# Optimization experiments

Hardware: AMD Instinct MI355X
Metric: run time of the kernel (lower is better)

Reference implementation:

```python
import jax, jax.numpy as jnp
import numpy as np

B, N, C = 32, 577, 768
H = 12
D = C // H
HID = 4 * C
EPS = 1e-5


def setup_inputs() -> dict:
    key = jax.random.key(0)
    ks = jax.random.split(key, 12)
    s = 0.02
    return {
        "x": jax.random.normal(ks[0], (B, N, C), dtype=jnp.float32),
        "ln1_g": jnp.ones((C,), jnp.float32),
        "ln1_b": jnp.zeros((C,), jnp.float32),
        "qkv_w": jax.random.normal(ks[1], (C, 3 * C), jnp.float32) * s,
        "qkv_b": jnp.zeros((3 * C,), jnp.float32),
        "proj_w": jax.random.normal(ks[2], (C, C), jnp.float32) * s,
        "proj_b": jnp.zeros((C,), jnp.float32),
        "ln2_g": jnp.ones((C,), jnp.float32),
        "ln2_b": jnp.zeros((C,), jnp.float32),
        "fc1_w": jax.random.normal(ks[3], (C, HID), jnp.float32) * s,
        "fc1_b": jnp.zeros((HID,), jnp.float32),
        "fc2_w": jax.random.normal(ks[4], (HID, C), jnp.float32) * s,
        "fc2_b": jnp.zeros((C,), jnp.float32),
    }


def _layernorm(x, g, b):
    mu = jnp.mean(x, axis=-1, keepdims=True)
    var = jnp.mean(jnp.square(x - mu), axis=-1, keepdims=True)
    return (x - mu) * jax.lax.rsqrt(var + EPS) * g + b


def reference(x, ln1_g, ln1_b, qkv_w, qkv_b, proj_w, proj_b,
              ln2_g, ln2_b, fc1_w, fc1_b, fc2_w, fc2_b):
    b, n, c = x.shape
    # --- MSA branch ---
    h = _layernorm(x, ln1_g, ln1_b)
    qkv = h @ qkv_w + qkv_b                      # [b, n, 3c]
    qkv = qkv.reshape(b, n, 3, H, D).transpose(2, 0, 3, 1, 4)  # [3, b, h, n, d]
    q, k, v = qkv[0], qkv[1], qkv[2]
    scale = D ** -0.5
    attn = jnp.einsum('bhqd,bhkd->bhqk', q, k) * scale
    attn = jax.nn.softmax(attn, axis=-1)
    o = jnp.einsum('bhqk,bhkd->bhqd', attn, v)   # [b, h, n, d]
    o = o.transpose(0, 2, 1, 3).reshape(b, n, c)
    o = o @ proj_w + proj_b
    x = x + o
    # --- MLP branch ---
    h = _layernorm(x, ln2_g, ln2_b)
    h = jax.nn.gelu(h @ fc1_w + fc1_b, approximate=False)  # torch nn.GELU = exact erf
    h = h @ fc2_w + fc2_b
    return x + h
```

## Files before the change

### kernel.cpp

```cpp
#include <hip/hip_runtime.h>

typedef unsigned short u16;
typedef short short8 __attribute__((ext_vector_type(8)));
typedef float f32x4 __attribute__((ext_vector_type(4)));

#define MM 18464
#define CC 768
#define NTOK 577

__device__ __forceinline__ u16 f2bf(float f) {
    unsigned u = __builtin_bit_cast(unsigned, f);
    u += 0x7fffu + ((u >> 16) & 1u);
    return (u16)(u >> 16);
}

__device__ __forceinline__ void gload16(const void* g, void* lds) {
    __builtin_amdgcn_global_load_lds(
        (const __attribute__((address_space(1))) unsigned*)g,
        (__attribute__((address_space(3))) unsigned*)lds,
        16, 0, 0);
}

__global__ __launch_bounds__(256) void convT(const float* __restrict__ src,
                                             u16* __restrict__ dst, int K, int N) {
    __shared__ float tile[32][33];
    const int k0 = blockIdx.x * 32, n0 = blockIdx.y * 32;
    const int tx = threadIdx.x & 31, ty = threadIdx.x >> 5;
#pragma unroll
    for (int i = 0; i < 32; i += 8)
        tile[ty + i][tx] = src[(size_t)(k0 + ty + i) * N + n0 + tx];
    __syncthreads();
#pragma unroll
    for (int i = 0; i < 32; i += 8)
        dst[(size_t)(n0 + ty + i) * K + k0 + tx] = f2bf(tile[tx][ty + i]);
}

__global__ __launch_bounds__(192) void ln_k(const float* __restrict__ x,
                                            const float* __restrict__ g,
                                            const float* __restrict__ bt,
                                            u16* __restrict__ out) {
    const int row = blockIdx.x, t = threadIdx.x;
    const float4 v = reinterpret_cast<const float4*>(x + (size_t)row * 768)[t];
    float s = v.x + v.y + v.z + v.w;
    float s2 = v.x * v.x + v.y * v.y + v.z * v.z + v.w * v.w;
#pragma unroll
    for (int off = 32; off > 0; off >>= 1) {
        s += __shfl_down(s, off);
        s2 += __shfl_down(s2, off);
    }
    __shared__ float red[6];
    if ((t & 63) == 0) { red[t >> 6] = s; red[3 + (t >> 6)] = s2; }
    __syncthreads();
    const float S = red[0] + red[1] + red[2];
    const float S2 = red[3] + red[4] + red[5];
    const float mu = S * (1.f / 768.f);
    const float var = S2 * (1.f / 768.f) - mu * mu;
    const float rs = rsqrtf(var + 1e-5f);
    const float4 gg = reinterpret_cast<const float4*>(g)[t];
    const float4 bb = reinterpret_cast<const float4*>(bt)[t];
    ushort4 r;
    r.x = f2bf((v.x - mu) * rs * gg.x + bb.x);
    r.y = f2bf((v.y - mu) * rs * gg.y + bb.y);
    r.z = f2bf((v.z - mu) * rs * gg.z + bb.z);
    r.w = f2bf((v.w - mu) * rs * gg.w + bb.w);
    reinterpret_cast<ushort4*>(out + (size_t)row * 768)[t] = r;
}

template <int MODE>
__global__ __launch_bounds__(256) void gemm_k(const u16* __restrict__ A,
                                              const u16* __restrict__ BT,
                                              const float* __restrict__ bias,
                                              const float* __restrict__ resid,
                                              void* __restrict__ outp,
                                              int M, int N, int K) {
    __shared__ u16 As[128 * 32];
    __shared__ u16 Bs[128 * 32];
    const int t = threadIdx.x;
    const int wid = t >> 6, lane = t & 63;
    const int l15 = lane & 15, lg = lane >> 4;
    const int m0 = blockIdx.x * 128, n0 = blockIdx.y * 128;
    const int wr = wid >> 1, wc = wid & 1;

    f32x4 acc[4][4] = {};

    const int srow = t >> 2;
    const int sk = (t & 3) * 8;
    const size_t a0 = (size_t)min(m0 + srow, M - 1) * K + sk;
    const size_t a1 = (size_t)min(m0 + srow + 64, M - 1) * K + sk;
    const size_t b0 = (size_t)(n0 + srow) * K + sk;
    const size_t b1 = (size_t)(n0 + srow + 64) * K + sk;
    u16* ldsA = As + wid * 512;
    u16* ldsB = Bs + wid * 512;

    for (int k0 = 0; k0 < K; k0 += 32) {
        gload16(A + a0 + k0, ldsA);
        gload16(A + a1 + k0, ldsA + 2048);
        gload16(BT + b0 + k0, ldsB);
        gload16(BT + b1 + k0, ldsB + 2048);
        __syncthreads();
        short8 af[4], bf[4];
#pragma unroll
        for (int fr = 0; fr < 4; ++fr)
            af[fr] = *(const short8*)&As[(wr * 64 + fr * 16 + l15) * 32 + lg * 8];
#pragma unroll
        for (int fc = 0; fc < 4; ++fc)
            bf[fc] = *(const short8*)&Bs[(wc * 64 + fc * 16 + l15) * 32 + lg * 8];
#pragma unroll
        for (int fr = 0; fr < 4; ++fr)
#pragma unroll
            for (int fc = 0; fc < 4; ++fc)
                acc[fr][fc] = __builtin_amdgcn_mfma_f32_16x16x32_bf16(
                    af[fr], bf[fc], acc[fr][fc], 0, 0, 0);
        __syncthreads();
    }

    float bcol[4];
#pragma unroll
    for (int fc = 0; fc < 4; ++fc) bcol[fc] = bias[n0 + wc * 64 + fc * 16 + l15];
#pragma unroll
    for (int fr = 0; fr < 4; ++fr) {
#pragma unroll
        for (int reg = 0; reg < 4; ++reg) {
            const int row = m0 + wr * 64 + fr * 16 + lg * 4 + reg;
            if (row < M) {
#pragma unroll
                for (int fc = 0; fc < 4; ++fc) {
                    const int col = n0 + wc * 64 + fc * 16 + l15;
                    float v = acc[fr][fc][reg] + bcol[fc];
                    if (MODE == 2) v = 0.5f * v * (1.0f + erff(v * 0.70710678118f));
                    if (MODE == 1 || MODE == 3) v += resid[(size_t)row * N + col];
                    if (MODE == 0 || MODE == 2)
                        ((u16*)outp)[(size_t)row * N + col] = f2bf(v);
                    else
                        ((float*)outp)[(size_t)row * N + col] = v;
                }
            }
        }
    }
}

__global__ __launch_bounds__(256) void attn_k(const u16* __restrict__ qkv,
                                              u16* __restrict__ o) {
    const int qt = blockIdx.x;
    const int bh = blockIdx.y;
    const int b = bh / 12, h = bh % 12;
    const int t = threadIdx.x, wid = t >> 6, lane = t & 63;
    const int l15 = lane & 15, lg = lane >> 4;
    const size_t base = ((size_t)b * NTOK) * 2304 + (size_t)h * 64;

    __shared__ u16 Ks[64 * 64], Vs[64 * 64], Ps[64 * 64];

    int qrow = qt * 64 + wid * 16 + l15;
    qrow = min(qrow, NTOK - 1);
    const u16* Qp = qkv + base + (size_t)qrow * 2304 + lg * 8;
    const short8 qf0 = *(const short8*)(Qp);
    const short8 qf1 = *(const short8*)(Qp + 32);

    f32x4 oacc[4] = {};
    float m_run[4], l_run[4];
#pragma unroll
    for (int j = 0; j < 4; ++j) { m_run[j] = -1e30f; l_run[j] = 0.f; }

    const int srow = t >> 3;
    const int sd = (t & 7) * 8;
    u16* ldsK = Ks + wid * 512;
    u16* ldsV = Vs + wid * 512;

    for (int kt = 0; kt < 10; ++kt) {
        const int n0t = kt * 64;
        const int r0 = min(n0t + srow, NTOK - 1);
        const int r1 = min(n0t + srow + 32, NTOK - 1);
        gload16(qkv + base + 768 + (size_t)r0 * 2304 + sd, ldsK);
        gload16(qkv + base + 768 + (size_t)r1 * 2304 + sd, ldsK + 2048);
        gload16(qkv + base + 1536 + (size_t)r0 * 2304 + sd, ldsV);
        gload16(qkv + base + 1536 + (size_t)r1 * 2304 + sd, ldsV + 2048);
        __syncthreads();

        f32x4 s[4];
#pragma unroll
        for (int fc = 0; fc < 4; ++fc) {
            f32x4 a_ = {};
            const short8 kf0 = *(const short8*)&Ks[(fc * 16 + l15) * 64 + lg * 8];
            const short8 kf1 = *(const short8*)&Ks[(fc * 16 + l15) * 64 + 32 + lg * 8];
            a_ = __builtin_amdgcn_mfma_f32_16x16x32_bf16(qf0, kf0, a_, 0, 0, 0);
            a_ = __builtin_amdgcn_mfma_f32_16x16x32_bf16(qf1, kf1, a_, 0, 0, 0);
            s[fc] = a_;
        }
#pragma unroll
        for (int fc = 0; fc < 4; ++fc) {
            const bool valid = (n0t + fc * 16 + l15) < NTOK;
#pragma unroll
            for (int j = 0; j < 4; ++j)
                s[fc][j] = valid ? s[fc][j] * 0.125f : -1e30f;
        }
        float mt[4];
#pragma unroll
        for (int j = 0; j < 4; ++j)
            mt[j] = fmaxf(fmaxf(s[0][j], s[1][j]), fmaxf(s[2][j], s[3][j]));
#pragma unroll
        for (int off = 1; off < 16; off <<= 1)
#pragma unroll
            for (int j = 0; j < 4; ++j) mt[j] = fmaxf(mt[j], __shfl_xor(mt[j], off));
        float mn[4], alpha[4];
#pragma unroll
        for (int j = 0; j < 4; ++j) {
            mn[j] = fmaxf(m_run[j], mt[j]);
            alpha[j] = __expf(m_run[j] - mn[j]);
            m_run[j] = mn[j];
        }
        float lsum[4] = {0.f, 0.f, 0.f, 0.f};
#pragma unroll
        for (int fc = 0; fc < 4; ++fc)
#pragma unroll
            for (int j = 0; j < 4; ++j) {
                const float p = __expf(s[fc][j] - mn[j]);
                s[fc][j] = p;
                lsum[j] += p;
            }
#pragma unroll
        for (int off = 1; off < 16; off <<= 1)
#pragma unroll
            for (int j = 0; j < 4; ++j) lsum[j] += __shfl_xor(lsum[j], off);
#pragma unroll
        for (int j = 0; j < 4; ++j) l_run[j] = l_run[j] * alpha[j] + lsum[j];
#pragma unroll
        for (int fc = 0; fc < 4; ++fc)
#pragma unroll
            for (int j = 0; j < 4; ++j) oacc[fc][j] *= alpha[j];

#pragma unroll
        for (int fc = 0; fc < 4; ++fc)
#pragma unroll
            for (int j = 0; j < 4; ++j)
                Ps[(wid * 16 + lg * 4 + j) * 64 + fc * 16 + l15] = f2bf(s[fc][j]);
        asm volatile("s_waitcnt lgkmcnt(0)" ::: "memory");

#pragma unroll
        for (int c = 0; c < 2; ++c) {
            const short8 pf = *(const short8*)&Ps[(wid * 16 + l15) * 64 + c * 32 + lg * 8];
#pragma unroll
            for (int fc = 0; fc < 4; ++fc) {
                short8 vf;
#pragma unroll
                for (int j = 0; j < 8; ++j)
                    vf[j] = (short)Vs[(c * 32 + lg * 8 + j) * 64 + fc * 16 + l15];
                oacc[fc] = __builtin_amdgcn_mfma_f32_16x16x32_bf16(pf, vf, oacc[fc], 0, 0, 0);
            }
        }
        __syncthreads();
    }

#pragma unroll
    for (int j = 0; j < 4; ++j) {
        const int row = qt * 64 + wid * 16 + lg * 4 + j;
        if (row < NTOK) {
            const float inv = 1.0f / l_run[j];
#pragma unroll
            for (int fc = 0; fc < 4; ++fc)
                o[((size_t)(b * NTOK + row)) * 768 + h * 64 + fc * 16 + l15] =
                    f2bf(oacc[fc][j] * inv);
        }
    }
}

extern "C" void kernel_launch(void* const* d_in, const int* in_sizes, int n_in,
                              void* d_out, int out_size, void* d_ws, size_t ws_size,
                              hipStream_t stream) {
    const float* x      = (const float*)d_in[0];
    const float* ln1_g  = (const float*)d_in[1];
    const float* ln1_b  = (const float*)d_in[2];
    const float* qkv_w  = (const float*)d_in[3];
    const float* qkv_b  = (const float*)d_in[4];
    const float* proj_w = (const float*)d_in[5];
    const float* proj_b = (const float*)d_in[6];
    const float* ln2_g  = (const float*)d_in[7];
    const float* ln2_b  = (const float*)d_in[8];
    const float* fc1_w  = (const float*)d_in[9];
    const float* fc1_b  = (const float*)d_in[10];
    const float* fc2_w  = (const float*)d_in[11];
    const float* fc2_b  = (const float*)d_in[12];
    float* out = (float*)d_out;

    char* ws = (char*)d_ws;
    size_t off = 0;
    u16* WQ  = (u16*)(ws + off); off += (size_t)2304 * 768 * 2;
    u16* WP  = (u16*)(ws + off); off += (size_t)768 * 768 * 2;
    u16* W1  = (u16*)(ws + off); off += (size_t)3072 * 768 * 2;
    u16* W2  = (u16*)(ws + off); off += (size_t)768 * 3072 * 2;
    u16* LN1 = (u16*)(ws + off); off += (size_t)MM * 768 * 2;
    u16* QKV = (u16*)(ws + off); off += (size_t)MM * 2304 * 2;
    u16* OB  = (u16*)(ws + off); off += (size_t)MM * 768 * 2;
    float* X1 = (float*)(ws + off); off += (size_t)MM * 768 * 4;
    u16* LN2 = (u16*)(ws + off); off += (size_t)MM * 768 * 2;
    u16* HID = LN1;

    convT<<<dim3(24, 72), 256, 0, stream>>>(qkv_w, WQ, 768, 2304);
    convT<<<dim3(24, 24), 256, 0, stream>>>(proj_w, WP, 768, 768);
    convT<<<dim3(24, 96), 256, 0, stream>>>(fc1_w, W1, 768, 3072);
    convT<<<dim3(96, 24), 256, 0, stream>>>(fc2_w, W2, 3072, 768);

    ln_k<<<MM, 192, 0, stream>>>(x, ln1_g, ln1_b, LN1);
    gemm_k<0><<<dim3(145, 18), 256, 0, stream>>>(LN1, WQ, qkv_b, nullptr, QKV,
                                                 MM, 2304, 768);
    attn_k<<<dim3(10, 384), 256, 0, stream>>>(QKV, OB);
    gemm_k<1><<<dim3(145, 6), 256, 0, stream>>>(OB, WP, proj_b, x, X1,
                                                MM, 768, 768);
    ln_k<<<MM, 192, 0, stream>>>(X1, ln2_g, ln2_b, LN2);
    gemm_k<2><<<dim3(145, 24), 256, 0, stream>>>(LN2, W1, fc1_b, nullptr, HID,
                                                 MM, 3072, 768);
    gemm_k<3><<<dim3(145, 6), 256, 0, stream>>>(HID, W2, fc2_b, X1, out,
                                                MM, 768, 3072);
}
```

Before: 891.8 us.

## Double-buffer GEMM LDS, add XCD swizzle, transpose V with XOR-swizzled attention LDS

The GEMM kernel now double-buffers its LDS tiles so the next K-slice's global-to-LDS load is issued before computing on the current slice. Both GEMM and attention remap block indices across the eight XCDs to improve L2 locality. In attention, K and P use XOR-swizzled LDS layouts to reduce bank conflicts, and V is stored transposed so the PV MFMA operand becomes a single 16-byte vector read instead of eight scalar LDS reads. The tradeoffs are twice the GEMM LDS footprint and V staging through registers rather than direct global-to-LDS loads.

```diff
diff --git a/kernel.cpp b/kernel.cpp
--- a/kernel.cpp
+++ b/kernel.cpp
@@ -5,7 +5,6 @@
 typedef float f32x4 __attribute__((ext_vector_type(4)));
 
 #define MM 18464
-#define CC 768
 #define NTOK 577
 
 __device__ __forceinline__ u16 f2bf(float f) {
@@ -19,6 +18,15 @@
         (const __attribute__((address_space(1))) unsigned*)g,
         (__attribute__((address_space(3))) unsigned*)lds,
         16, 0, 0);
+}
+
+__device__ __forceinline__ int2 xcd_swz(int gx, int gy) {
+    const int nwg = gx * gy;
+    const int flat = blockIdx.x + blockIdx.y * gx;
+    const int q = nwg >> 3, r = nwg & 7;
+    const int xcd = flat & 7, lid = flat >> 3;
+    const int w = (xcd < r ? xcd * (q + 1) : r * (q + 1) + (xcd - r) * q) + lid;
+    int2 o; o.x = w % gx; o.y = w / gx; return o;
 }
 
 __global__ __launch_bounds__(256) void convT(const float* __restrict__ src,
@@ -73,12 +81,13 @@
                                               const float* __restrict__ resid,
                                               void* __restrict__ outp,
                                               int M, int N, int K) {
-    __shared__ u16 As[128 * 32];
-    __shared__ u16 Bs[128 * 32];
+    __shared__ u16 As[2][128 * 32];
+    __shared__ u16 Bs[2][128 * 32];
     const int t = threadIdx.x;
     const int wid = t >> 6, lane = t & 63;
     const int l15 = lane & 15, lg = lane >> 4;
-    const int m0 = blockIdx.x * 128, n0 = blockIdx.y * 128;
+    const int2 sw = xcd_swz(gridDim.x, gridDim.y);
+    const int m0 = sw.x * 128, n0 = sw.y * 128;
     const int wr = wid >> 1, wc = wid & 1;
 
     f32x4 acc[4][4] = {};
@@ -89,30 +98,41 @@
     const size_t a1 = (size_t)min(m0 + srow + 64, M - 1) * K + sk;
     const size_t b0 = (size_t)(n0 + srow) * K + sk;
     const size_t b1 = (size_t)(n0 + srow + 64) * K + sk;
-    u16* ldsA = As + wid * 512;
-    u16* ldsB = Bs + wid * 512;
-
-    for (int k0 = 0; k0 < K; k0 += 32) {
-        gload16(A + a0 + k0, ldsA);
-        gload16(A + a1 + k0, ldsA + 2048);
-        gload16(BT + b0 + k0, ldsB);
-        gload16(BT + b1 + k0, ldsB + 2048);
-        __syncthreads();
-        short8 af[4], bf[4];
+    const int wo = wid * 512;
+
+    auto stage = [&](int buf, int k0) {
+        gload16(A + a0 + k0, &As[buf][wo]);
+        gload16(A + a1 + k0, &As[buf][wo + 2048]);
+        gload16(BT + b0 + k0, &Bs[buf][wo]);
+        gload16(BT + b1 + k0, &Bs[buf][wo + 2048]);
+    };
+    auto compute = [&](int buf) {
+        short8 af[4], bfr[4];
 #pragma unroll
         for (int fr = 0; fr < 4; ++fr)
-            af[fr] = *(const short8*)&As[(wr * 64 + fr * 16 + l15) * 32 + lg * 8];
+            af[fr] = *(const short8*)&As[buf][(wr * 64 + fr * 16 + l15) * 32 + lg * 8];
 #pragma unroll
         for (int fc = 0; fc < 4; ++fc)
-            bf[fc] = *(const short8*)&Bs[(wc * 64 + fc * 16 + l15) * 32 + lg * 8];
+            bfr[fc] = *(const short8*)&Bs[buf][(wc * 64 + fc * 16 + l15) * 32 + lg * 8];
 #pragma unroll
         for (int fr = 0; fr < 4; ++fr)
 #pragma unroll
             for (int fc = 0; fc < 4; ++fc)
                 acc[fr][fc] = __builtin_amdgcn_mfma_f32_16x16x32_bf16(
-                    af[fr], bf[fc], acc[fr][fc], 0, 0, 0);
+                    af[fr], bfr[fc], acc[fr][fc], 0, 0, 0);
+    };
+
+    stage(0, 0);
+    __syncthreads();
+    int cur = 0;
+    const int nk = K >> 5;
+    for (int kt = 1; kt < nk; ++kt) {
+        stage(cur ^ 1, kt * 32);
+        compute(cur);
         __syncthreads();
-    }
+        cur ^= 1;
+    }
+    compute(cur);
 
     float bcol[4];
 #pragma unroll
@@ -141,14 +161,15 @@
 
 __global__ __launch_bounds__(256) void attn_k(const u16* __restrict__ qkv,
                                               u16* __restrict__ o) {
-    const int qt = blockIdx.x;
-    const int bh = blockIdx.y;
+    const int2 sw = xcd_swz(10, 384);
+    const int qt = sw.x;
+    const int bh = sw.y;
     const int b = bh / 12, h = bh % 12;
     const int t = threadIdx.x, wid = t >> 6, lane = t & 63;
     const int l15 = lane & 15, lg = lane >> 4;
     const size_t base = ((size_t)b * NTOK) * 2304 + (size_t)h * 64;
 
-    __shared__ u16 Ks[64 * 64], Vs[64 * 64], Ps[64 * 64];
+    __shared__ u16 Ks[64 * 64], VT[64 * 64], Ps[64 * 64];
 
     int qrow = qt * 64 + wid * 16 + l15;
     qrow = min(qrow, NTOK - 1);
@@ -162,26 +183,34 @@
     for (int j = 0; j < 4; ++j) { m_run[j] = -1e30f; l_run[j] = 0.f; }
 
     const int srow = t >> 3;
-    const int sd = (t & 7) * 8;
+    const int cchunk = t & 7;
+    const int ksd = (cchunk ^ (srow & 7)) * 8;
     u16* ldsK = Ks + wid * 512;
-    u16* ldsV = Vs + wid * 512;
+    const int vs0 = ((srow >> 3) ^ cchunk) * 8 + (srow & 7);
+    const int vs1 = (((srow >> 3) + 4) ^ cchunk) * 8 + (srow & 7);
 
     for (int kt = 0; kt < 10; ++kt) {
         const int n0t = kt * 64;
         const int r0 = min(n0t + srow, NTOK - 1);
         const int r1 = min(n0t + srow + 32, NTOK - 1);
-        gload16(qkv + base + 768 + (size_t)r0 * 2304 + sd, ldsK);
-        gload16(qkv + base + 768 + (size_t)r1 * 2304 + sd, ldsK + 2048);
-        gload16(qkv + base + 1536 + (size_t)r0 * 2304 + sd, ldsV);
-        gload16(qkv + base + 1536 + (size_t)r1 * 2304 + sd, ldsV + 2048);
+        gload16(qkv + base + 768 + (size_t)r0 * 2304 + ksd, ldsK);
+        gload16(qkv + base + 768 + (size_t)r1 * 2304 + ksd, ldsK + 2048);
+        const short8 v0 = *(const short8*)(qkv + base + 1536 + (size_t)r0 * 2304 + cchunk * 8);
+        const short8 v1 = *(const short8*)(qkv + base + 1536 + (size_t)r1 * 2304 + cchunk * 8);
+#pragma unroll
+        for (int j = 0; j < 8; ++j) {
+            VT[(cchunk * 8 + j) * 64 + vs0] = (u16)v0[j];
+            VT[(cchunk * 8 + j) * 64 + vs1] = (u16)v1[j];
+        }
         __syncthreads();
 
         f32x4 s[4];
 #pragma unroll
         for (int fc = 0; fc < 4; ++fc) {
+            const int krow = fc * 16 + l15;
+            const short8 kf0 = *(const short8*)&Ks[krow * 64 + ((lg ^ (krow & 7)) * 8)];
+            const short8 kf1 = *(const short8*)&Ks[krow * 64 + (((lg + 4) ^ (krow & 7)) * 8)];
             f32x4 a_ = {};
-            const short8 kf0 = *(const short8*)&Ks[(fc * 16 + l15) * 64 + lg * 8];
-            const short8 kf1 = *(const short8*)&Ks[(fc * 16 + l15) * 64 + 32 + lg * 8];
             a_ = __builtin_amdgcn_mfma_f32_16x16x32_bf16(qf0, kf0, a_, 0, 0, 0);
             a_ = __builtin_amdgcn_mfma_f32_16x16x32_bf16(qf1, kf1, a_, 0, 0, 0);
             s[fc] = a_;
@@ -231,19 +260,22 @@
 #pragma unroll
         for (int fc = 0; fc < 4; ++fc)
 #pragma unroll
-            for (int j = 0; j < 4; ++j)
-                Ps[(wid * 16 + lg * 4 + j) * 64 + fc * 16 + l15] = f2bf(s[fc][j]);
+            for (int j = 0; j < 4; ++j) {
+                const int q = wid * 16 + lg * 4 + j;
+                Ps[q * 64 + (((fc * 2 + (l15 >> 3)) ^ (q & 7)) * 8) + (l15 & 7)] =
+                    f2bf(s[fc][j]);
+            }
         asm volatile("s_waitcnt lgkmcnt(0)" ::: "memory");
 
 #pragma unroll
         for (int c = 0; c < 2; ++c) {
-            const short8 pf = *(const short8*)&Ps[(wid * 16 + l15) * 64 + c * 32 + lg * 8];
+            const short8 pf = *(const short8*)
+                &Ps[(wid * 16 + l15) * 64 + (((c * 4 + lg) ^ (l15 & 7)) * 8)];
 #pragma unroll
             for (int fc = 0; fc < 4; ++fc) {
-                short8 vf;
-#pragma unroll
-                for (int j = 0; j < 8; ++j)
-                    vf[j] = (short)Vs[(c * 32 + lg * 8 + j) * 64 + fc * 16 + l15];
+                const short8 vf = *(const short8*)
+                    &VT[(fc * 16 + l15) * 64 +
+                        (((c * 4 + lg) ^ (fc * 2 + (l15 >> 3))) * 8)];
                 oacc[fc] = __builtin_amdgcn_mfma_f32_16x16x32_bf16(pf, vf, oacc[fc], 0, 0, 0);
             }
         }
```

After: 849.2 us. 4.8% less time.
